# Performance work log

Hardware: AMD Instinct MI355X
Metric: run time of the kernel (lower is better)

## Reference

```python
import jax, jax.numpy as jnp
import numpy as np

N = 100000      # nodes
E = 1000000     # edges per relation
D_IN = 128
D_OUT = 128
SLOPE = 0.2
N_REL = 3


def setup_inputs() -> dict:
    key = jax.random.key(0)
    ks = jax.random.split(key, 1 + 4 * N_REL)
    inp = {"H": jax.random.normal(ks[0], (N, D_IN), dtype=jnp.float32)}
    xav_w = float(np.sqrt(6.0 / (D_IN + D_OUT)))   # xavier_uniform bound for W
    xav_a = float(np.sqrt(6.0 / (1 + 2 * D_OUT)))  # xavier_uniform on a viewed as [1, 2d]
    for i in range(N_REL):
        inp[f"row_{i}"] = jax.random.randint(ks[1 + 4 * i], (E,), 0, N, dtype=jnp.int64)
        inp[f"col_{i}"] = jax.random.randint(ks[2 + 4 * i], (E,), 0, N, dtype=jnp.int64)
        inp[f"W_{i}"] = jax.random.uniform(ks[3 + 4 * i], (D_IN, D_OUT), jnp.float32, -xav_w, xav_w)
        inp[f"a_{i}"] = jax.random.uniform(ks[4 + 4 * i], (2 * D_OUT,), jnp.float32, -xav_a, xav_a)
    inp["bias"] = jnp.zeros((D_OUT,), jnp.float32)
    return inp


def _relation_agg(H, W, a, row, col):
    # 1) transform: Wh = H @ W_r  [N, d]
    Wh = H @ W
    d = Wh.shape[1]
    # 2) edge scores: e_ij = leaky_relu(a[:d].Wh[row] + a[d:].Wh[col])
    s_dst = Wh @ a[:d]   # coefficient for destination (row) side  [N]
    s_src = Wh @ a[d:]   # coefficient for source (col) side       [N]
    e = jax.nn.leaky_relu(s_dst[row] + s_src[col], negative_slope=SLOPE)  # [E]
    # 3) segment softmax over incoming edges of each destination node
    e_max = jax.ops.segment_max(e, row, num_segments=N)          # [N]
    e_shift = jnp.exp(e - e_max[row])                            # [E]
    e_sum = jax.ops.segment_sum(e_shift, row, num_segments=N)    # [N]
    alpha = e_shift / jnp.maximum(e_sum[row], 1e-12)             # [E]
    # 4) weighted aggregation of source features
    return jax.ops.segment_sum(alpha[:, None] * Wh[col], row, num_segments=N)  # [N, d]


def reference(H, row_0, col_0, row_1, col_1, row_2, col_2,
              W_0, W_1, W_2, a_0, a_1, a_2, bias):
    rows = (row_0, row_1, row_2)
    cols = (col_0, col_1, col_2)
    Ws = (W_0, W_1, W_2)
    As = (a_0, a_1, a_2)
    agg = jnp.zeros((N, D_OUT), H.dtype)
    for r in range(N_REL):
        agg = agg + _relation_agg(H, Ws[r], As[r], rows[r], cols[r])
    return agg + bias
```

## Files before the change

kernel.cpp:

```cpp
#include <hip/hip_runtime.h>

#define SLOPE 0.2f

typedef unsigned int uint;
typedef unsigned short ushort;
typedef __attribute__((ext_vector_type(8))) short short8;
typedef __attribute__((ext_vector_type(4))) float f32x4;

#define BINW 2048
#define BINSHIFT 11
#define CAP 22528

__device__ inline ushort f2bf(float f) {
    uint u = __float_as_uint(f);
    uint r = (u + 0x7FFFu + ((u >> 16) & 1u)) >> 16;
    return (ushort)r;
}
__device__ inline uint pack2bf(float lo, float hi) {
    return (uint)f2bf(lo) | ((uint)f2bf(hi) << 16);
}
__device__ inline float bfl(uint u) { return __uint_as_float(u << 16); }
__device__ inline float bfh(uint u) { return __uint_as_float(u & 0xFFFF0000u); }

__global__ void wt3(const float* __restrict__ W0, const float* __restrict__ W1,
                    const float* __restrict__ W2,
                    const float* __restrict__ a0, const float* __restrict__ a1,
                    const float* __restrict__ a2,
                    ushort* __restrict__ WT, float* __restrict__ wa,
                    int* __restrict__ bincnt, int nbz) {
    int r = blockIdx.x;
    if (r == 0 && threadIdx.x < nbz) bincnt[threadIdx.x] = 0;
    const float* W = (r == 0) ? W0 : (r == 1) ? W1 : W2;
    const float* a = (r == 0) ? a0 : (r == 1) ? a1 : a2;
    ushort* wt = WT + r * 16384;
    for (int i = threadIdx.x; i < 16384; i += 256) {
        int k = i >> 7, n = i & 127;
        wt[n * 128 + k] = f2bf(W[i]);
    }
    if (threadIdx.x < 128) {
        int k = threadIdx.x;
        const float* wrow = W + k * 128;
        float pd = 0.f, ps = 0.f;
        for (int n = 0; n < 128; n += 4) {
            float4 w4 = *reinterpret_cast<const float4*>(wrow + n);
            float4 aL = *reinterpret_cast<const float4*>(a + n);
            float4 aR = *reinterpret_cast<const float4*>(a + 128 + n);
            pd += w4.x * aL.x + w4.y * aL.y + w4.z * aL.z + w4.w * aL.w;
            ps += w4.x * aR.x + w4.y * aR.y + w4.z * aR.z + w4.w * aR.w;
        }
        wa[r * 256 + k] = pd;
        wa[r * 256 + 128 + k] = ps;
    }
}

__global__ __launch_bounds__(256) void gemm3(const float* __restrict__ H,
                                             const ushort* __restrict__ WT,
                                             ushort* __restrict__ whAll, int N) {
    __shared__ ushort lds[16384];
    const int brow = blockIdx.x * 128;
    const int t = threadIdx.x;

    for (int c = t; c < 2048; c += 256) {
        int r = c >> 4;
        int kb = (c & 15) << 4;
        int gr = brow + r;
        uint4 u = make_uint4(0, 0, 0, 0);
        if (gr < N) {
            const float* hp = H + (size_t)gr * 128 + (kb >> 1);
            float4 v0 = *reinterpret_cast<const float4*>(hp);
            float4 v1 = *reinterpret_cast<const float4*>(hp + 4);
            u.x = pack2bf(v0.x, v0.y);
            u.y = pack2bf(v0.z, v0.w);
            u.z = pack2bf(v1.x, v1.y);
            u.w = pack2bf(v1.z, v1.w);
        }
        int dst = (r << 8) + (kb ^ ((r & 7) << 4));
        *reinterpret_cast<uint4*>((char*)lds + dst) = u;
    }
    __syncthreads();

    const int wave = t >> 6, lane = t & 63;
    const int l16 = lane & 15, lhi = lane >> 4;

    for (int rel = 0; rel < 3; ++rel) {
        ushort* Wh = whAll + (size_t)rel * N * 128;
        const ushort* wt = WT + rel * 16384;

        short8 bf[2][4];
#pragma unroll
        for (int nt = 0; nt < 2; ++nt) {
            int n = wave * 32 + nt * 16 + l16;
#pragma unroll
            for (int ks = 0; ks < 4; ++ks)
                bf[nt][ks] = *reinterpret_cast<const short8*>(wt + n * 128 + ks * 32 + lhi * 8);
        }

        f32x4 acc[8][2];
#pragma unroll
        for (int mt = 0; mt < 8; ++mt) { acc[mt][0] = (f32x4)(0.f); acc[mt][1] = (f32x4)(0.f); }

#pragma unroll
        for (int ks = 0; ks < 4; ++ks) {
#pragma unroll
            for (int mt = 0; mt < 8; ++mt) {
                int r = mt * 16 + l16;
                int kb = (ks * 32 + lhi * 8) * 2;
                int addr = (r << 8) + (kb ^ ((r & 7) << 4));
                short8 af = *reinterpret_cast<const short8*>((char*)lds + addr);
                acc[mt][0] = __builtin_amdgcn_mfma_f32_16x16x32_bf16(af, bf[0][ks], acc[mt][0], 0, 0, 0);
                acc[mt][1] = __builtin_amdgcn_mfma_f32_16x16x32_bf16(af, bf[1][ks], acc[mt][1], 0, 0, 0);
            }
        }

#pragma unroll
        for (int mt = 0; mt < 8; ++mt)
#pragma unroll
            for (int nt = 0; nt < 2; ++nt)
#pragma unroll
                for (int reg = 0; reg < 4; ++reg) {
                    int gr = brow + mt * 16 + lhi * 4 + reg;
                    if (gr < N)
                        Wh[(size_t)gr * 128 + wave * 32 + nt * 16 + l16] = f2bf(acc[mt][nt][reg]);
                }
    }
}

__global__ __launch_bounds__(256) void scores_k(const float* __restrict__ H,
                                                const float* __restrict__ wa,
                                                float* __restrict__ sd,
                                                float* __restrict__ ss, int N) {
    int node = blockIdx.x * 16 + (threadIdx.x >> 4);
    int ql = threadIdx.x & 15;
    if (node >= N) return;
    const float* hp = H + (size_t)node * 128 + ql * 8;
    float4 h0 = *reinterpret_cast<const float4*>(hp);
    float4 h1 = *reinterpret_cast<const float4*>(hp + 4);
#pragma unroll
    for (int r = 0; r < 3; ++r) {
        const float* wd = wa + r * 256 + ql * 8;
        const float* wsv = wa + r * 256 + 128 + ql * 8;
        float4 d0 = *reinterpret_cast<const float4*>(wd);
        float4 d1 = *reinterpret_cast<const float4*>(wd + 4);
        float4 s0 = *reinterpret_cast<const float4*>(wsv);
        float4 s1 = *reinterpret_cast<const float4*>(wsv + 4);
        float pd = h0.x * d0.x + h0.y * d0.y + h0.z * d0.z + h0.w * d0.w +
                   h1.x * d1.x + h1.y * d1.y + h1.z * d1.z + h1.w * d1.w;
        float ps = h0.x * s0.x + h0.y * s0.y + h0.z * s0.z + h0.w * s0.w +
                   h1.x * s1.x + h1.y * s1.y + h1.z * s1.z + h1.w * s1.w;
#pragma unroll
        for (int off = 1; off < 16; off <<= 1) {
            pd += __shfl_xor(pd, off);
            ps += __shfl_xor(ps, off);
        }
        if (ql == 0) { sd[r * N + node] = pd; ss[r * N + node] = ps; }
    }
}

__global__ __launch_bounds__(256) void binscatter(const int* __restrict__ r0, const int* __restrict__ r1,
                                                  const int* __restrict__ r2, const int* __restrict__ c0,
                                                  const int* __restrict__ c1, const int* __restrict__ c2,
                                                  const float* __restrict__ sd, const float* __restrict__ ss,
                                                  int* __restrict__ bincnt, uint2* __restrict__ binned,
                                                  int E, int N, int nbins) {
    __shared__ uint2 staged[4096];
    __shared__ int hist[256], sB[256], curi[256], gbase[256];
    const int t = threadIdx.x;
    hist[t] = 0;
    __syncthreads();

    uint2 rec[16];
    short bn[16];
    const int base = blockIdx.x * 4096;
#pragma unroll
    for (int k = 0; k < 16; ++k) {
        int i = base + k * 256 + t;
        bn[k] = -1;
        if (i < 3 * E) {
            int r = (i >= 2 * E) ? 2 : (i >= E) ? 1 : 0;
            int li = i - r * E;
            const int* rp = (r == 0) ? r0 : (r == 1) ? r1 : r2;
            const int* cp = (r == 0) ? c0 : (r == 1) ? c1 : c2;
            int rr = __builtin_nontemporal_load(rp + li);
            int cc = __builtin_nontemporal_load(cp + li);
            int idx = r * N + rr;
            int b = idx >> BINSHIFT;
            uint lo = (uint)(idx & (BINW - 1));
            float x = sd[idx] + ss[r * N + cc];
            x = (x > 0.f) ? x : SLOPE * x;
            float w = __expf(x);
            rec[k] = make_uint2((uint)cc | (lo << 17), __float_as_uint(w));
            bn[k] = (short)b;
            atomicAdd(&hist[b], 1);
        }
    }
    __syncthreads();

    int v = hist[t];
    int* pa = hist; int* pb = sB;
    for (int off = 1; off < 256; off <<= 1) {
        int x = pa[t] + ((t >= off) ? pa[t - off] : 0);
        pb[t] = x;
        __syncthreads();
        int* tmp = pa; pa = pb; pb = tmp;
    }
    sB[t] = pa[t] - v;
    curi[t] = pa[t] - v;
    if (t < nbins && v > 0) gbase[t] = t * CAP + atomicAdd(&bincnt[t], v);
    __syncthreads();

#pragma unroll
    for (int k = 0; k < 16; ++k)
        if (bn[k] >= 0) {
            int p = atomicAdd(&curi[bn[k]], 1);
            staged[p] = rec[k];
        }
    __syncthreads();

    const int g32 = t >> 5, lane32 = t & 31;
    for (int b = g32; b < nbins; b += 8) {
        int s = sB[b];
        int len = hist[b] - s;
        if (len <= 0) continue;
        int g = gbase[b];
        for (int j = lane32; j < len; j += 32) binned[g + j] = staged[s + j];
    }
}

__global__ __launch_bounds__(256) void binscan(const int* __restrict__ bincnt,
                                               int* __restrict__ binbase, int nbins) {
    __shared__ int sA[256], sB[256];
    int t = threadIdx.x;
    int v = (t < nbins) ? bincnt[t] : 0;
    sA[t] = v;
    __syncthreads();
    int* pa = sA; int* pb = sB;
    for (int off = 1; off < 256; off <<= 1) {
        int x = pa[t] + ((t >= off) ? pa[t - off] : 0);
        pb[t] = x;
        __syncthreads();
        int* tmp = pa; pa = pb; pb = tmp;
    }
    if (t < nbins) binbase[t] = pa[t] - v;
    if (t == nbins - 1) binbase[nbins] = pa[t];
}

__global__ __launch_bounds__(256) void binsort(const uint2* __restrict__ binned,
                                               const int* __restrict__ bincnt,
                                               const int* __restrict__ binbase,
                                               uint2* __restrict__ wc, int* __restrict__ offs,
                                               int L, int N) {
    __shared__ int s1[BINW];
    __shared__ int wsum[4];
    const int b = blockIdx.x, t = threadIdx.x;
    const int cnt = bincnt[b];
    const int dst0 = binbase[b];
    const uint2* src = binned + (size_t)b * CAP;
    const int ibase = b << BINSHIFT;
    const int width = min(BINW, L - ibase);

    for (int i = t; i < BINW; i += 256) s1[i] = 0;
    __syncthreads();
    for (int j = t; j < cnt; j += 256)
        atomicAdd(&s1[(src[j].x >> 17) & (BINW - 1)], 1);
    __syncthreads();

    const int cb = t * 8;
    int v[8];
    int run = 0;
#pragma unroll
    for (int k = 0; k < 8; ++k) { run += s1[cb + k]; v[k] = run; }
    const int lane = t & 63, wv = t >> 6;
    int x = run;
#pragma unroll
    for (int off = 1; off < 64; off <<= 1) {
        int y = __shfl_up(x, off);
        if (lane >= off) x += y;
    }
    if (lane == 63) wsum[wv] = x;
    __syncthreads();
    int pre = x - run;
#pragma unroll
    for (int w = 0; w < 3; ++w) if (wv > w) pre += wsum[w];

#pragma unroll
    for (int k = 0; k < 8; ++k) {
        int i = cb + k;
        if (i < width) offs[ibase + i] = dst0 + pre + v[k];
    }
#pragma unroll
    for (int k = 0; k < 8; ++k)
        s1[cb + k] = dst0 + pre + (k ? v[k - 1] : 0);
    __syncthreads();

    for (int j = t; j < cnt; j += 256) {
        uint2 r = src[j];
        uint lo = (r.x >> 17) & (BINW - 1);
        int p = atomicAdd(&s1[lo], 1);
        int gidx = ibase + (int)lo;
        int rel = (gidx >= 2 * N) ? 2 : (gidx >= N) ? 1 : 0;
        uint cc = r.x & 0x1FFFFu;
        wc[p] = make_uint2(r.y, (uint)(rel * N) + cc);
    }
}

__global__ __launch_bounds__(256) void aggregate3(const uint* __restrict__ whAll,
                                                  const uint2* __restrict__ wc,
                                                  const int* __restrict__ offs,
                                                  const float* __restrict__ bias,
                                                  float* __restrict__ out, int N) {
    int node = blockIdx.x * 16 + (threadIdx.x >> 4);
    int ql = threadIdx.x & 15;
    if (node >= N) return;

    float t0 = 0.f, t1 = 0.f, t2 = 0.f, t3 = 0.f, t4 = 0.f, t5 = 0.f, t6 = 0.f, t7 = 0.f;

#pragma unroll
    for (int r = 0; r < 3; ++r) {
        int idx = r * N + node;
        int end = offs[idx];
        int beg = (idx == 0) ? 0 : offs[idx - 1];
        if (beg >= end) continue;

        float wsA = 0.f, wsB = 0.f;
        float a0 = 0.f, a1 = 0.f, a2 = 0.f, a3 = 0.f, a4 = 0.f, a5 = 0.f, a6 = 0.f, a7 = 0.f;
        float g0 = 0.f, g1 = 0.f, g2 = 0.f, g3 = 0.f, g4 = 0.f, g5 = 0.f, g6 = 0.f, g7 = 0.f;

        int j = beg;
        for (; j + 4 <= end; j += 4) {
            uint2 e0 = wc[j], e1 = wc[j + 1], e2 = wc[j + 2], e3 = wc[j + 3];
            uint4 v0 = reinterpret_cast<const uint4*>(whAll + ((size_t)e0.y << 6))[ql];
            uint4 v1 = reinterpret_cast<const uint4*>(whAll + ((size_t)e1.y << 6))[ql];
            uint4 v2 = reinterpret_cast<const uint4*>(whAll + ((size_t)e2.y << 6))[ql];
            uint4 v3 = reinterpret_cast<const uint4*>(whAll + ((size_t)e3.y << 6))[ql];
            float w0 = __uint_as_float(e0.x), w1 = __uint_as_float(e1.x);
            float w2 = __uint_as_float(e2.x), w3 = __uint_as_float(e3.x);
            wsA += w0 + w2;
            wsB += w1 + w3;
            a0 = fmaf(w0, bfl(v0.x), a0); a1 = fmaf(w0, bfh(v0.x), a1);
            a2 = fmaf(w0, bfl(v0.y), a2); a3 = fmaf(w0, bfh(v0.y), a3);
            a4 = fmaf(w0, bfl(v0.z), a4); a5 = fmaf(w0, bfh(v0.z), a5);
            a6 = fmaf(w0, bfl(v0.w), a6); a7 = fmaf(w0, bfh(v0.w), a7);
            g0 = fmaf(w1, bfl(v1.x), g0); g1 = fmaf(w1, bfh(v1.x), g1);
            g2 = fmaf(w1, bfl(v1.y), g2); g3 = fmaf(w1, bfh(v1.y), g3);
            g4 = fmaf(w1, bfl(v1.z), g4); g5 = fmaf(w1, bfh(v1.z), g5);
            g6 = fmaf(w1, bfl(v1.w), g6); g7 = fmaf(w1, bfh(v1.w), g7);
            a0 = fmaf(w2, bfl(v2.x), a0); a1 = fmaf(w2, bfh(v2.x), a1);
            a2 = fmaf(w2, bfl(v2.y), a2); a3 = fmaf(w2, bfh(v2.y), a3);
            a4 = fmaf(w2, bfl(v2.z), a4); a5 = fmaf(w2, bfh(v2.z), a5);
            a6 = fmaf(w2, bfl(v2.w), a6); a7 = fmaf(w2, bfh(v2.w), a7);
            g0 = fmaf(w3, bfl(v3.x), g0); g1 = fmaf(w3, bfh(v3.x), g1);
            g2 = fmaf(w3, bfl(v3.y), g2); g3 = fmaf(w3, bfh(v3.y), g3);
            g4 = fmaf(w3, bfl(v3.z), g4); g5 = fmaf(w3, bfh(v3.z), g5);
            g6 = fmaf(w3, bfl(v3.w), g6); g7 = fmaf(w3, bfh(v3.w), g7);
        }
        for (; j < end; ++j) {
            uint2 e = wc[j];
            float w = __uint_as_float(e.x);
            uint4 v = reinterpret_cast<const uint4*>(whAll + ((size_t)e.y << 6))[ql];
            wsA += w;
            a0 = fmaf(w, bfl(v.x), a0); a1 = fmaf(w, bfh(v.x), a1);
            a2 = fmaf(w, bfl(v.y), a2); a3 = fmaf(w, bfh(v.y), a3);
            a4 = fmaf(w, bfl(v.z), a4); a5 = fmaf(w, bfh(v.z), a5);
            a6 = fmaf(w, bfl(v.w), a6); a7 = fmaf(w, bfh(v.w), a7);
        }
        float inv = 1.f / fmaxf(wsA + wsB, 1e-12f);
        t0 = fmaf(a0 + g0, inv, t0); t1 = fmaf(a1 + g1, inv, t1);
        t2 = fmaf(a2 + g2, inv, t2); t3 = fmaf(a3 + g3, inv, t3);
        t4 = fmaf(a4 + g4, inv, t4); t5 = fmaf(a5 + g5, inv, t5);
        t6 = fmaf(a6 + g6, inv, t6); t7 = fmaf(a7 + g7, inv, t7);
    }

    float4 b0 = *reinterpret_cast<const float4*>(bias + ql * 8);
    float4 b1 = *reinterpret_cast<const float4*>(bias + ql * 8 + 4);
    float* o = out + (size_t)node * 128 + ql * 8;
    f32x4 o0 = {t0 + b0.x, t1 + b0.y, t2 + b0.z, t3 + b0.w};
    f32x4 o1 = {t4 + b1.x, t5 + b1.y, t6 + b1.z, t7 + b1.w};
    __builtin_nontemporal_store(o0, reinterpret_cast<f32x4*>(o));
    __builtin_nontemporal_store(o1, reinterpret_cast<f32x4*>(o + 4));
}

extern "C" void kernel_launch(void* const* d_in, const int* in_sizes, int n_in,
                              void* d_out, int out_size, void* d_ws, size_t ws_size,
                              hipStream_t stream) {
    const float* H = (const float*)d_in[0];
    const int* row[3] = {(const int*)d_in[1], (const int*)d_in[5], (const int*)d_in[9]};
    const int* col[3] = {(const int*)d_in[2], (const int*)d_in[6], (const int*)d_in[10]};
    const float* W[3] = {(const float*)d_in[3], (const float*)d_in[7], (const float*)d_in[11]};
    const float* a[3] = {(const float*)d_in[4], (const float*)d_in[8], (const float*)d_in[12]};
    const float* bias = (const float*)d_in[13];

    const int N = in_sizes[0] / 128;
    const int E = in_sizes[1];
    float* out = (float*)d_out;

    const int L = 3 * N;
    const int nbins = (L + BINW - 1) >> BINSHIFT;

    char* ws = (char*)d_ws;
    size_t off = 0;
    auto alloc = [&](size_t bytes) -> void* {
        void* p = ws + off;
        off += (bytes + 255) & ~(size_t)255;
        return p;
    };

    ushort* WT = (ushort*)alloc(3 * 16384 * 2);
    float* wa = (float*)alloc(3 * 256 * 4);
    ushort* whAll = (ushort*)alloc((size_t)3 * N * 128 * 2);
    float* sd = (float*)alloc((size_t)L * 4);
    float* ss = (float*)alloc((size_t)L * 4);
    int* offs = (int*)alloc((size_t)L * 4);
    int* bincnt = (int*)alloc((size_t)(nbins + 2) * 4);
    int* binbase = (int*)alloc((size_t)(nbins + 2) * 4);
    uint2* wc = (uint2*)alloc((size_t)3 * E * 8);
    uint2* binned = (uint2*)d_out;

    const int nbG = (N + 127) / 128;
    const int nbQ = (N + 15) / 16;
    const int nbB = (3 * E + 4095) / 4096;

    wt3<<<3, 256, 0, stream>>>(W[0], W[1], W[2], a[0], a[1], a[2], WT, wa, bincnt, nbins + 2);
    gemm3<<<nbG, 256, 0, stream>>>(H, WT, whAll, N);
    scores_k<<<nbQ, 256, 0, stream>>>(H, wa, sd, ss, N);

    binscatter<<<nbB, 256, 0, stream>>>(row[0], row[1], row[2], col[0], col[1], col[2],
                                        sd, ss, bincnt, binned, E, N, nbins);
    binscan<<<1, 256, 0, stream>>>(bincnt, binbase, nbins);
    binsort<<<nbins, 256, 0, stream>>>(binned, bincnt, binbase, wc, offs, L, N);

    aggregate3<<<nbQ, 256, 0, stream>>>((const uint*)whAll, wc, offs, bias, out, N);
}
```

Before: 283.7 us.

## Interleave relations per node, normalize softmax in binsort, fuse gemm/scores and binscan

The segment index becomes node*3+rel instead of rel*N+node, so all three relations of a node sit contiguously in the sorted edge list. The aggregate kernel can then walk them as one range. Softmax denominators are computed in binsort with shared-memory float atomics and folded into the stored edge weights, which removes the per-relation division loop from aggregation. The scores kernel is merged into the GEMM launch as extra blocks, and the single-block bin scan is recomputed redundantly inside each binsort block. Together these remove two launches, at the cost of float atomics in LDS and a modulo in binsort.

```diff
diff --git a/kernel.cpp b/kernel.cpp
--- a/kernel.cpp
+++ b/kernel.cpp
@@ -53,12 +53,45 @@
     }
 }
 
-__global__ __launch_bounds__(256) void gemm3(const float* __restrict__ H,
-                                             const ushort* __restrict__ WT,
-                                             ushort* __restrict__ whAll, int N) {
+__global__ __launch_bounds__(256) void gemm_scores(const float* __restrict__ H,
+                                                   const ushort* __restrict__ WT,
+                                                   const float* __restrict__ wa,
+                                                   ushort* __restrict__ whAll,
+                                                   float* __restrict__ sd,
+                                                   float* __restrict__ ss, int N, int nbG) {
     __shared__ ushort lds[16384];
+    const int t = threadIdx.x;
+
+    if ((int)blockIdx.x >= nbG) {
+        int node = ((int)blockIdx.x - nbG) * 16 + (t >> 4);
+        int ql = t & 15;
+        if (node >= N) return;
+        const float* hp = H + (size_t)node * 128 + ql * 8;
+        float4 h0 = *reinterpret_cast<const float4*>(hp);
+        float4 h1 = *reinterpret_cast<const float4*>(hp + 4);
+#pragma unroll
+        for (int r = 0; r < 3; ++r) {
+            const float* wd = wa + r * 256 + ql * 8;
+            const float* wsv = wa + r * 256 + 128 + ql * 8;
+            float4 d0 = *reinterpret_cast<const float4*>(wd);
+            float4 d1 = *reinterpret_cast<const float4*>(wd + 4);
+            float4 s0 = *reinterpret_cast<const float4*>(wsv);
+            float4 s1 = *reinterpret_cast<const float4*>(wsv + 4);
+            float pd = h0.x * d0.x + h0.y * d0.y + h0.z * d0.z + h0.w * d0.w +
+                       h1.x * d1.x + h1.y * d1.y + h1.z * d1.z + h1.w * d1.w;
+            float ps = h0.x * s0.x + h0.y * s0.y + h0.z * s0.z + h0.w * s0.w +
+                       h1.x * s1.x + h1.y * s1.y + h1.z * s1.z + h1.w * s1.w;
+#pragma unroll
+            for (int off = 1; off < 16; off <<= 1) {
+                pd += __shfl_xor(pd, off);
+                ps += __shfl_xor(ps, off);
+            }
+            if (ql == 0) { sd[r * N + node] = pd; ss[r * N + node] = ps; }
+        }
+        return;
+    }
+
     const int brow = blockIdx.x * 128;
-    const int t = threadIdx.x;
 
     for (int c = t; c < 2048; c += 256) {
         int r = c >> 4;
@@ -125,37 +158,6 @@
     }
 }
 
-__global__ __launch_bounds__(256) void scores_k(const float* __restrict__ H,
-                                                const float* __restrict__ wa,
-                                                float* __restrict__ sd,
-                                                float* __restrict__ ss, int N) {
-    int node = blockIdx.x * 16 + (threadIdx.x >> 4);
-    int ql = threadIdx.x & 15;
-    if (node >= N) return;
-    const float* hp = H + (size_t)node * 128 + ql * 8;
-    float4 h0 = *reinterpret_cast<const float4*>(hp);
-    float4 h1 = *reinterpret_cast<const float4*>(hp + 4);
-#pragma unroll
-    for (int r = 0; r < 3; ++r) {
-        const float* wd = wa + r * 256 + ql * 8;
-        const float* wsv = wa + r * 256 + 128 + ql * 8;
-        float4 d0 = *reinterpret_cast<const float4*>(wd);
-        float4 d1 = *reinterpret_cast<const float4*>(wd + 4);
-        float4 s0 = *reinterpret_cast<const float4*>(wsv);
-        float4 s1 = *reinterpret_cast<const float4*>(wsv + 4);
-        float pd = h0.x * d0.x + h0.y * d0.y + h0.z * d0.z + h0.w * d0.w +
-                   h1.x * d1.x + h1.y * d1.y + h1.z * d1.z + h1.w * d1.w;
-        float ps = h0.x * s0.x + h0.y * s0.y + h0.z * s0.z + h0.w * s0.w +
-                   h1.x * s1.x + h1.y * s1.y + h1.z * s1.z + h1.w * s1.w;
-#pragma unroll
-        for (int off = 1; off < 16; off <<= 1) {
-            pd += __shfl_xor(pd, off);
-            ps += __shfl_xor(ps, off);
-        }
-        if (ql == 0) { sd[r * N + node] = pd; ss[r * N + node] = ps; }
-    }
-}
-
 __global__ __launch_bounds__(256) void binscatter(const int* __restrict__ r0, const int* __restrict__ r1,
                                                   const int* __restrict__ r2, const int* __restrict__ c0,
                                                   const int* __restrict__ c1, const int* __restrict__ c2,
@@ -182,10 +184,10 @@
             const int* cp = (r == 0) ? c0 : (r == 1) ? c1 : c2;
             int rr = __builtin_nontemporal_load(rp + li);
             int cc = __builtin_nontemporal_load(cp + li);
-            int idx = r * N + rr;
+            int idx = rr * 3 + r;
             int b = idx >> BINSHIFT;
             uint lo = (uint)(idx & (BINW - 1));
-            float x = sd[idx] + ss[r * N + cc];
+            float x = sd[r * N + rr] + ss[r * N + cc];
             x = (x > 0.f) ? x : SLOPE * x;
             float w = __expf(x);
             rec[k] = make_uint2((uint)cc | (lo << 17), __float_as_uint(w));
@@ -226,43 +228,45 @@
     }
 }
 
-__global__ __launch_bounds__(256) void binscan(const int* __restrict__ bincnt,
-                                               int* __restrict__ binbase, int nbins) {
-    __shared__ int sA[256], sB[256];
-    int t = threadIdx.x;
-    int v = (t < nbins) ? bincnt[t] : 0;
-    sA[t] = v;
-    __syncthreads();
-    int* pa = sA; int* pb = sB;
+__global__ __launch_bounds__(256) void binsort(const uint2* __restrict__ binned,
+                                               const int* __restrict__ bincnt,
+                                               uint2* __restrict__ wc, int* __restrict__ offs,
+                                               int L, int N, int nbins) {
+    __shared__ int s1[BINW];
+    __shared__ float fsum[BINW];
+    __shared__ int wsum4[4];
+    __shared__ int sc[256], sc2[256];
+    const int b = blockIdx.x, t = threadIdx.x;
+
+    int bv = (t < nbins) ? bincnt[t] : 0;
+    sc[t] = bv;
+    __syncthreads();
+    int* pa = sc; int* pb = sc2;
     for (int off = 1; off < 256; off <<= 1) {
         int x = pa[t] + ((t >= off) ? pa[t - off] : 0);
         pb[t] = x;
         __syncthreads();
         int* tmp = pa; pa = pb; pb = tmp;
     }
-    if (t < nbins) binbase[t] = pa[t] - v;
-    if (t == nbins - 1) binbase[nbins] = pa[t];
-}
-
-__global__ __launch_bounds__(256) void binsort(const uint2* __restrict__ binned,
-                                               const int* __restrict__ bincnt,
-                                               const int* __restrict__ binbase,
-                                               uint2* __restrict__ wc, int* __restrict__ offs,
-                                               int L, int N) {
-    __shared__ int s1[BINW];
-    __shared__ int wsum[4];
-    const int b = blockIdx.x, t = threadIdx.x;
+    __shared__ int sh_dst0;
+    if (t == b) sh_dst0 = pa[t] - bv;
+    __syncthreads();
+    const int dst0 = sh_dst0;
     const int cnt = bincnt[b];
-    const int dst0 = binbase[b];
     const uint2* src = binned + (size_t)b * CAP;
     const int ibase = b << BINSHIFT;
     const int width = min(BINW, L - ibase);
 
-    for (int i = t; i < BINW; i += 256) s1[i] = 0;
-    __syncthreads();
-    for (int j = t; j < cnt; j += 256)
-        atomicAdd(&s1[(src[j].x >> 17) & (BINW - 1)], 1);
-    __syncthreads();
+    for (int i = t; i < BINW; i += 256) { s1[i] = 0; fsum[i] = 0.f; }
+    __syncthreads();
+    for (int j = t; j < cnt; j += 256) {
+        uint2 r = src[j];
+        uint lo = (r.x >> 17) & (BINW - 1);
+        atomicAdd(&s1[lo], 1);
+        atomicAdd(&fsum[lo], __uint_as_float(r.y));
+    }
+    __syncthreads();
+    for (int i = t; i < BINW; i += 256) fsum[i] = 1.f / fmaxf(fsum[i], 1e-12f);
 
     const int cb = t * 8;
     int v[8];
@@ -276,11 +280,11 @@
         int y = __shfl_up(x, off);
         if (lane >= off) x += y;
     }
-    if (lane == 63) wsum[wv] = x;
+    if (lane == 63) wsum4[wv] = x;
     __syncthreads();
     int pre = x - run;
 #pragma unroll
-    for (int w = 0; w < 3; ++w) if (wv > w) pre += wsum[w];
+    for (int w = 0; w < 3; ++w) if (wv > w) pre += wsum4[w];
 
 #pragma unroll
     for (int k = 0; k < 8; ++k) {
@@ -295,11 +299,12 @@
     for (int j = t; j < cnt; j += 256) {
         uint2 r = src[j];
         uint lo = (r.x >> 17) & (BINW - 1);
+        float wn = __uint_as_float(r.y) * fsum[lo];
         int p = atomicAdd(&s1[lo], 1);
         int gidx = ibase + (int)lo;
-        int rel = (gidx >= 2 * N) ? 2 : (gidx >= N) ? 1 : 0;
+        int rel = gidx - (gidx / 3) * 3;
         uint cc = r.x & 0x1FFFFu;
-        wc[p] = make_uint2(r.y, (uint)(rel * N) + cc);
+        wc[p] = make_uint2(__float_as_uint(wn), (uint)(rel * N) + cc);
     }
 }
 
@@ -312,69 +317,54 @@
     int ql = threadIdx.x & 15;
     if (node >= N) return;
 
-    float t0 = 0.f, t1 = 0.f, t2 = 0.f, t3 = 0.f, t4 = 0.f, t5 = 0.f, t6 = 0.f, t7 = 0.f;
-
-#pragma unroll
-    for (int r = 0; r < 3; ++r) {
-        int idx = r * N + node;
-        int end = offs[idx];
-        int beg = (idx == 0) ? 0 : offs[idx - 1];
-        if (beg >= end) continue;
-
-        float wsA = 0.f, wsB = 0.f;
-        float a0 = 0.f, a1 = 0.f, a2 = 0.f, a3 = 0.f, a4 = 0.f, a5 = 0.f, a6 = 0.f, a7 = 0.f;
-        float g0 = 0.f, g1 = 0.f, g2 = 0.f, g3 = 0.f, g4 = 0.f, g5 = 0.f, g6 = 0.f, g7 = 0.f;
-
-        int j = beg;
-        for (; j + 4 <= end; j += 4) {
-            uint2 e0 = wc[j], e1 = wc[j + 1], e2 = wc[j + 2], e3 = wc[j + 3];
-            uint4 v0 = reinterpret_cast<const uint4*>(whAll + ((size_t)e0.y << 6))[ql];
-            uint4 v1 = reinterpret_cast<const uint4*>(whAll + ((size_t)e1.y << 6))[ql];
-            uint4 v2 = reinterpret_cast<const uint4*>(whAll + ((size_t)e2.y << 6))[ql];
-            uint4 v3 = reinterpret_cast<const uint4*>(whAll + ((size_t)e3.y << 6))[ql];
-            float w0 = __uint_as_float(e0.x), w1 = __uint_as_float(e1.x);
-            float w2 = __uint_as_float(e2.x), w3 = __uint_as_float(e3.x);
-            wsA += w0 + w2;
-            wsB += w1 + w3;
-            a0 = fmaf(w0, bfl(v0.x), a0); a1 = fmaf(w0, bfh(v0.x), a1);
-            a2 = fmaf(w0, bfl(v0.y), a2); a3 = fmaf(w0, bfh(v0.y), a3);
-            a4 = fmaf(w0, bfl(v0.z), a4); a5 = fmaf(w0, bfh(v0.z), a5);
-            a6 = fmaf(w0, bfl(v0.w), a6); a7 = fmaf(w0, bfh(v0.w), a7);
-            g0 = fmaf(w1, bfl(v1.x), g0); g1 = fmaf(w1, bfh(v1.x), g1);
-            g2 = fmaf(w1, bfl(v1.y), g2); g3 = fmaf(w1, bfh(v1.y), g3);
-            g4 = fmaf(w1, bfl(v1.z), g4); g5 = fmaf(w1, bfh(v1.z), g5);
-            g6 = fmaf(w1, bfl(v1.w), g6); g7 = fmaf(w1, bfh(v1.w), g7);
-            a0 = fmaf(w2, bfl(v2.x), a0); a1 = fmaf(w2, bfh(v2.x), a1);
-            a2 = fmaf(w2, bfl(v2.y), a2); a3 = fmaf(w2, bfh(v2.y), a3);
-            a4 = fmaf(w2, bfl(v2.z), a4); a5 = fmaf(w2, bfh(v2.z), a5);
-            a6 = fmaf(w2, bfl(v2.w), a6); a7 = fmaf(w2, bfh(v2.w), a7);
-            g0 = fmaf(w3, bfl(v3.x), g0); g1 = fmaf(w3, bfh(v3.x), g1);
-            g2 = fmaf(w3, bfl(v3.y), g2); g3 = fmaf(w3, bfh(v3.y), g3);
-            g4 = fmaf(w3, bfl(v3.z), g4); g5 = fmaf(w3, bfh(v3.z), g5);
-            g6 = fmaf(w3, bfl(v3.w), g6); g7 = fmaf(w3, bfh(v3.w), g7);
-        }
-        for (; j < end; ++j) {
-            uint2 e = wc[j];
-            float w = __uint_as_float(e.x);
-            uint4 v = reinterpret_cast<const uint4*>(whAll + ((size_t)e.y << 6))[ql];
-            wsA += w;
-            a0 = fmaf(w, bfl(v.x), a0); a1 = fmaf(w, bfh(v.x), a1);
-            a2 = fmaf(w, bfl(v.y), a2); a3 = fmaf(w, bfh(v.y), a3);
-            a4 = fmaf(w, bfl(v.z), a4); a5 = fmaf(w, bfh(v.z), a5);
-            a6 = fmaf(w, bfl(v.w), a6); a7 = fmaf(w, bfh(v.w), a7);
-        }
-        float inv = 1.f / fmaxf(wsA + wsB, 1e-12f);
-        t0 = fmaf(a0 + g0, inv, t0); t1 = fmaf(a1 + g1, inv, t1);
-        t2 = fmaf(a2 + g2, inv, t2); t3 = fmaf(a3 + g3, inv, t3);
-        t4 = fmaf(a4 + g4, inv, t4); t5 = fmaf(a5 + g5, inv, t5);
-        t6 = fmaf(a6 + g6, inv, t6); t7 = fmaf(a7 + g7, inv, t7);
+    const int b3 = node * 3;
+    int beg = (b3 == 0) ? 0 : offs[b3 - 1];
+    const int end = offs[b3 + 2];
+
+    float a0 = 0.f, a1 = 0.f, a2 = 0.f, a3 = 0.f, a4 = 0.f, a5 = 0.f, a6 = 0.f, a7 = 0.f;
+    float g0 = 0.f, g1 = 0.f, g2 = 0.f, g3 = 0.f, g4 = 0.f, g5 = 0.f, g6 = 0.f, g7 = 0.f;
+
+    int j = beg;
+    for (; j + 4 <= end; j += 4) {
+        uint2 e0 = wc[j], e1 = wc[j + 1], e2 = wc[j + 2], e3 = wc[j + 3];
+        uint4 v0 = reinterpret_cast<const uint4*>(whAll + ((size_t)e0.y << 6))[ql];
+        uint4 v1 = reinterpret_cast<const uint4*>(whAll + ((size_t)e1.y << 6))[ql];
+        uint4 v2 = reinterpret_cast<const uint4*>(whAll + ((size_t)e2.y << 6))[ql];
+        uint4 v3 = reinterpret_cast<const uint4*>(whAll + ((size_t)e3.y << 6))[ql];
+        float w0 = __uint_as_float(e0.x), w1 = __uint_as_float(e1.x);
+        float w2 = __uint_as_float(e2.x), w3 = __uint_as_float(e3.x);
+        a0 = fmaf(w0, bfl(v0.x), a0); a1 = fmaf(w0, bfh(v0.x), a1);
+        a2 = fmaf(w0, bfl(v0.y), a2); a3 = fmaf(w0, bfh(v0.y), a3);
+        a4 = fmaf(w0, bfl(v0.z), a4); a5 = fmaf(w0, bfh(v0.z), a5);
+        a6 = fmaf(w0, bfl(v0.w), a6); a7 = fmaf(w0, bfh(v0.w), a7);
+        g0 = fmaf(w1, bfl(v1.x), g0); g1 = fmaf(w1, bfh(v1.x), g1);
+        g2 = fmaf(w1, bfl(v1.y), g2); g3 = fmaf(w1, bfh(v1.y), g3);
+        g4 = fmaf(w1, bfl(v1.z), g4); g5 = fmaf(w1, bfh(v1.z), g5);
+        g6 = fmaf(w1, bfl(v1.w), g6); g7 = fmaf(w1, bfh(v1.w), g7);
+        a0 = fmaf(w2, bfl(v2.x), a0); a1 = fmaf(w2, bfh(v2.x), a1);
+        a2 = fmaf(w2, bfl(v2.y), a2); a3 = fmaf(w2, bfh(v2.y), a3);
+        a4 = fmaf(w2, bfl(v2.z), a4); a5 = fmaf(w2, bfh(v2.z), a5);
+        a6 = fmaf(w2, bfl(v2.w), a6); a7 = fmaf(w2, bfh(v2.w), a7);
+        g0 = fmaf(w3, bfl(v3.x), g0); g1 = fmaf(w3, bfh(v3.x), g1);
+        g2 = fmaf(w3, bfl(v3.y), g2); g3 = fmaf(w3, bfh(v3.y), g3);
+        g4 = fmaf(w3, bfl(v3.z), g4); g5 = fmaf(w3, bfh(v3.z), g5);
+        g6 = fmaf(w3, bfl(v3.w), g6); g7 = fmaf(w3, bfh(v3.w), g7);
+    }
+    for (; j < end; ++j) {
+        uint2 e = wc[j];
+        float w = __uint_as_float(e.x);
+        uint4 v = reinterpret_cast<const uint4*>(whAll + ((size_t)e.y << 6))[ql];
+        a0 = fmaf(w, bfl(v.x), a0); a1 = fmaf(w, bfh(v.x), a1);
+        a2 = fmaf(w, bfl(v.y), a2); a3 = fmaf(w, bfh(v.y), a3);
+        a4 = fmaf(w, bfl(v.z), a4); a5 = fmaf(w, bfh(v.z), a5);
+        a6 = fmaf(w, bfl(v.w), a6); a7 = fmaf(w, bfh(v.w), a7);
     }
 
     float4 b0 = *reinterpret_cast<const float4*>(bias + ql * 8);
     float4 b1 = *reinterpret_cast<const float4*>(bias + ql * 8 + 4);
     float* o = out + (size_t)node * 128 + ql * 8;
-    f32x4 o0 = {t0 + b0.x, t1 + b0.y, t2 + b0.z, t3 + b0.w};
-    f32x4 o1 = {t4 + b1.x, t5 + b1.y, t6 + b1.z, t7 + b1.w};
+    f32x4 o0 = {a0 + g0 + b0.x, a1 + g1 + b0.y, a2 + g2 + b0.z, a3 + g3 + b0.w};
+    f32x4 o1 = {a4 + g4 + b1.x, a5 + g5 + b1.y, a6 + g6 + b1.z, a7 + g7 + b1.w};
     __builtin_nontemporal_store(o0, reinterpret_cast<f32x4*>(o));
     __builtin_nontemporal_store(o1, reinterpret_cast<f32x4*>(o + 4));
 }
@@ -411,7 +401,6 @@
     float* ss = (float*)alloc((size_t)L * 4);
     int* offs = (int*)alloc((size_t)L * 4);
     int* bincnt = (int*)alloc((size_t)(nbins + 2) * 4);
-    int* binbase = (int*)alloc((size_t)(nbins + 2) * 4);
     uint2* wc = (uint2*)alloc((size_t)3 * E * 8);
     uint2* binned = (uint2*)d_out;
 
@@ -420,13 +409,11 @@
     const int nbB = (3 * E + 4095) / 4096;
 
     wt3<<<3, 256, 0, stream>>>(W[0], W[1], W[2], a[0], a[1], a[2], WT, wa, bincnt, nbins + 2);
-    gemm3<<<nbG, 256, 0, stream>>>(H, WT, whAll, N);
-    scores_k<<<nbQ, 256, 0, stream>>>(H, wa, sd, ss, N);
+    gemm_scores<<<nbG + nbQ, 256, 0, stream>>>(H, WT, wa, whAll, sd, ss, N, nbG);
 
     binscatter<<<nbB, 256, 0, stream>>>(row[0], row[1], row[2], col[0], col[1], col[2],
                                         sd, ss, bincnt, binned, E, N, nbins);
-    binscan<<<1, 256, 0, stream>>>(bincnt, binbase, nbins);
-    binsort<<<nbins, 256, 0, stream>>>(binned, bincnt, binbase, wc, offs, L, N);
+    binsort<<<nbins, 256, 0, stream>>>(binned, bincnt, wc, offs, L, N, nbins);
 
     aggregate3<<<nbQ, 256, 0, stream>>>((const uint*)whAll, wc, offs, bias, out, N);
 }
```

Result: slower. 304.1 us (+7.2%).
